# Performance work log

Measured on AMD Instinct MI355X. Metric: run time of the kernel, lower is better.

The kernel has to match this reference:

```python
import jax, jax.numpy as jnp
import numpy as np

K = 512
DIM = 64


def setup_inputs() -> dict:
    key = jax.random.key(0)
    kx, ke = jax.random.split(key)
    x = jax.random.normal(kx, (64, 64, 32, 32), dtype=jnp.float32)  # (b, d, h, w)
    codebook = jax.random.normal(ke, (K, DIM), dtype=jnp.float32)  # nn.Embedding weight
    return {"x": x, "codebook": codebook}


def reference(x, codebook):
    b, d, h, w = x.shape
    # (b, d, h*w) -> (b, h*w, d)
    flat = jnp.transpose(x.reshape(b, d, h * w), (0, 2, 1))  # (b, n, d)
    x2 = jnp.sum(flat * flat, axis=-1, keepdims=True)              # (b, n, 1)
    e2 = jnp.sum(codebook * codebook, axis=-1)                     # (k,)
    xe = jnp.einsum('bnd,kd->bnk', flat, codebook)                 # (b, n, k)
    dist = x2 - 2.0 * xe + e2                                      # (b, n, k)
    idx = jnp.argmin(dist, axis=-1)                                # (b, n)
    quant = codebook[idx]                                          # (b, n, d) gather
    # straight-through estimator
    quant_st = flat + jax.lax.stop_gradient(quant - flat)
    out = jnp.transpose(quant_st, (0, 2, 1)).reshape(b, d, h, w)
    return out
```

## Files before the change

### kernel.cpp

```cpp
#include <hip/hip_runtime.h>

#define KCODES 512
#define DIM    64
#define NVEC   65536
#define TAU    0.05f

typedef __attribute__((ext_vector_type(8))) short   short8;
typedef __attribute__((ext_vector_type(4))) float   f32x4;

static __device__ __forceinline__ unsigned f2bfu(float f) {
    unsigned u = __builtin_bit_cast(unsigned, f);
    u += 0x7fffu + ((u >> 16) & 1u);
    return u >> 16;
}

__global__ void prep_kernel(const float* __restrict__ cb,
                            unsigned short* __restrict__ cbt,
                            float* __restrict__ e2q) {
    if (blockIdx.x < 128) {
        const int g   = blockIdx.x * 64 + threadIdx.x;
        const int s   = g >> 10;
        const int rem = g & 1023;
        const int h   = rem >> 9;
        const int qd  = (rem >> 6) & 7;
        const int cl  = rem & 63;
        const float* src = cb + (size_t)(s * 64 + cl) * DIM + qd * 8;
        short8 v;
#pragma unroll
        for (int j = 0; j < 8; ++j) {
            float f = src[j];
            unsigned u = __builtin_bit_cast(unsigned, f);
            if (h == 0) {
                v[j] = (short)(u >> 16);
            } else {
                float hi = __builtin_bit_cast(float, u & 0xFFFF0000u);
                v[j] = (short)f2bfu(f - hi);
            }
        }
        *(short8*)(cbt + (size_t)g * 8) = v;
    } else {
        const int k = blockIdx.x - 128;
        float v = cb[k * DIM + threadIdx.x];
        double p = (double)v * (double)v;
#pragma unroll
        for (int off = 32; off > 0; off >>= 1) p += __shfl_down(p, off, 64);
        if (threadIdx.x == 0) e2q[k] = (float)(0.5 * p + 256.0);
    }
}

__launch_bounds__(256, 4)
__global__ void vq_main(const float* __restrict__ x,
                        const float* __restrict__ cb,
                        const unsigned short* __restrict__ cbt,
                        const float* __restrict__ e2q,
                        float* __restrict__ out) {
    __shared__ __align__(16) unsigned short sA[2][8192];
    __shared__ float sE2[KCODES];
    __shared__ int   s_i1[64], s_i2[64], s_flag[64], s_win[64];

    const int tid  = threadIdx.x;
    const int wave = tid >> 6;
    const int lane = tid & 63;
    const int quad = lane >> 4;
    const int l16  = lane & 15;

    const int v0    = blockIdx.x * 64;
    const int b     = v0 >> 10;
    const int nbase = v0 & 1023;
    const float* xb = x + (size_t)b * 65536;

    short8 stg[4];
#pragma unroll
    for (int r = 0; r < 4; ++r)
        stg[r] = *(const short8*)(cbt + (size_t)(tid + r * 256) * 8);

    short8 Bh[2], Bl[2];
    {
        const int n_g = nbase + wave * 16 + l16;
#pragma unroll
        for (int ko = 0; ko < 2; ++ko) {
#pragma unroll
            for (int j = 0; j < 8; ++j) {
                const int d = quad * 8 + j + ko * 32;
                float f = -xb[(size_t)d * 1024 + n_g];
                unsigned u = __builtin_bit_cast(unsigned, f);
                float hi = __builtin_bit_cast(float, u & 0xFFFF0000u);
                Bh[ko][j] = (short)(u >> 16);
                Bl[ko][j] = (short)f2bfu(f - hi);
            }
        }
    }

    if (tid < 128) *(f32x4*)(sE2 + tid * 4) = *(const f32x4*)(e2q + tid * 4);
#pragma unroll
    for (int r = 0; r < 4; ++r)
        *(short8*)(sA[0] + (size_t)(tid + r * 256) * 8) = stg[r];
    __syncthreads();

    float f1 = 1e30f, f2_ = 1e30f;
    int   i1 = 0,     i2_ = 0;

#pragma unroll 1
    for (int s = 0; s < 8; ++s) {
        if (s < 7) {
#pragma unroll
            for (int r = 0; r < 4; ++r)
                stg[r] = *(const short8*)(cbt +
                          (size_t)((s + 1) * 1024 + tid + r * 256) * 8);
        }

        const unsigned short* buf = sA[s & 1];
#pragma unroll
        for (int st = 0; st < 4; ++st) {
            const int cbase = s * 64 + st * 16;
            const int roff  = quad * 64 + st * 16 + l16;
            short8 A00 = *(const short8*)(buf + (size_t)(      roff) * 8);
            short8 A01 = *(const short8*)(buf + (size_t)(256 + roff) * 8);
            short8 A10 = *(const short8*)(buf + (size_t)(512 + roff) * 8);
            short8 A11 = *(const short8*)(buf + (size_t)(768 + roff) * 8);
            f32x4  e2v = *(const f32x4*)(sE2 + cbase + quad * 4);

            f32x4 acc = e2v;
            acc = __builtin_amdgcn_mfma_f32_16x16x32_bf16(A00, Bh[0], acc, 0, 0, 0);
            acc = __builtin_amdgcn_mfma_f32_16x16x32_bf16(A01, Bh[1], acc, 0, 0, 0);
            acc = __builtin_amdgcn_mfma_f32_16x16x32_bf16(A00, Bl[0], acc, 0, 0, 0);
            acc = __builtin_amdgcn_mfma_f32_16x16x32_bf16(A01, Bl[1], acc, 0, 0, 0);
            acc = __builtin_amdgcn_mfma_f32_16x16x32_bf16(A10, Bh[0], acc, 0, 0, 0);
            acc = __builtin_amdgcn_mfma_f32_16x16x32_bf16(A11, Bh[1], acc, 0, 0, 0);

#pragma unroll
            for (int r = 0; r < 4; ++r) {
                float dd = acc[r];
                int   id = cbase + quad * 4 + r;
                bool  c1 = dd < f1;
                bool  c2 = dd < f2_;
                i2_ = c1 ? i1 : (c2 ? id : i2_);
                f2_ = fminf(fmaxf(f1, dd), f2_);
                i1  = c1 ? id : i1;
                f1  = fminf(f1, dd);
            }
        }

        if (s < 7) {
#pragma unroll
            for (int r = 0; r < 4; ++r)
                *(short8*)(sA[(s + 1) & 1] + (size_t)(tid + r * 256) * 8) = stg[r];
        }
        __syncthreads();
    }

    {
#pragma unroll
        for (int delta = 16; delta <= 32; delta <<= 1) {
            float of1 = __shfl_xor(f1, delta, 64);
            int   oi1 = __shfl_xor(i1, delta, 64);
            float of2 = __shfl_xor(f2_, delta, 64);
            int   oi2 = __shfl_xor(i2_, delta, 64);
            bool o1_first = (of1 < f1) || (of1 == f1 && oi1 < i1);
            if (o1_first) {
                bool keep = (f1 < of2) || (f1 == of2 && i1 < oi2);
                f2_ = keep ? f1 : of2;
                i2_ = keep ? i1 : oi2;
                f1 = of1; i1 = oi1;
            } else {
                bool o1_second = (of1 < f2_) || (of1 == f2_ && oi1 < i2_);
                if (o1_second) { f2_ = of1; i2_ = oi1; }
            }
        }
        if (quad == 0) {
            const int vl = wave * 16 + l16;
            s_win[vl]  = i1;
            s_i1[vl]   = i1;
            s_i2[vl]   = i2_;
            s_flag[vl] = (f2_ - f1) < TAU;
        }
    }
    __syncthreads();

    {
        const int vec = tid >> 2, sub = tid & 3;
        if (s_flag[vec]) {
            const int i1c = s_i1[vec], i2c = s_i2[vec];
            const float* xr = xb + nbase + vec;
            const float* r1 = cb + (size_t)i1c * DIM;
            const float* r2 = cb + (size_t)i2c * DIM;
            double D1 = 0.0, D2 = 0.0;
#pragma unroll 4
            for (int i = 0; i < 16; ++i) {
                const int d = sub + 4 * i;
                double xd = (double)xr[(size_t)d * 1024];
                double t1 = xd - (double)r1[d]; D1 += t1 * t1;
                double t2 = xd - (double)r2[d]; D2 += t2 * t2;
            }
            D1 += __shfl_down(D1, 2, 64); D1 += __shfl_down(D1, 1, 64);
            D2 += __shfl_down(D2, 2, 64); D2 += __shfl_down(D2, 1, 64);
            if (sub == 0) {
                if (D2 < D1 || (D2 == D1 && i2c < i1c)) s_win[vec] = i2c;
            }
        }
    }
    __syncthreads();

    {
        const int n    = tid & 63;
        const int dgrp = tid >> 6;
        const float4* crow = (const float4*)(cb + (size_t)s_win[n] * DIM);
        float* op = out + (size_t)b * 65536 + nbase + n;
#pragma unroll
        for (int i = 0; i < 4; ++i) {
            const int d0 = dgrp * 16 + i * 4;
            float4 val = crow[d0 >> 2];
            op[(size_t)(d0 + 0) * 1024] = val.x;
            op[(size_t)(d0 + 1) * 1024] = val.y;
            op[(size_t)(d0 + 2) * 1024] = val.z;
            op[(size_t)(d0 + 3) * 1024] = val.w;
        }
    }
}

extern "C" void kernel_launch(void* const* d_in, const int* in_sizes, int n_in,
                              void* d_out, int out_size, void* d_ws, size_t ws_size,
                              hipStream_t stream) {
    const float* x  = (const float*)d_in[0];
    const float* cb = (const float*)d_in[1];
    float* out = (float*)d_out;

    unsigned short* cbt = (unsigned short*)d_ws;
    float*          e2q = (float*)(cbt + 8192 * 8);

    prep_kernel<<<640, 64, 0, stream>>>(cb, cbt, e2q);
    vq_main<<<NVEC / 64, 256, 0, stream>>>(x, cb, cbt, e2q, out);
}
```

Measured before the change: 89.73 us.

## Split codebook across waves so each wave handles all 64 vectors

Each wave now owns a 16-code slice of every 64-code stage and computes distances for all four 16-vector tiles, with the x fragments shared through LDS. Each A fragment read from LDS is reused across four MFMA groups, so per-wave LDS reads of the codebook drop roughly fourfold. Because each wave now sees only a quarter of the codes, the per-vector top-2 results from the four waves are merged in a cross-wave LDS reduction stage. The cost is more registers (launch bounds lowered from 4 to 3 blocks per CU), 16KB of extra shared memory, and an extra barrier with a serial merge step.

```diff
diff --git a/kernel.cpp b/kernel.cpp
--- a/kernel.cpp
+++ b/kernel.cpp
@@ -48,15 +48,25 @@
     }
 }
 
-__launch_bounds__(256, 4)
+__launch_bounds__(256, 3)
 __global__ void vq_main(const float* __restrict__ x,
                         const float* __restrict__ cb,
                         const unsigned short* __restrict__ cbt,
                         const float* __restrict__ e2q,
                         float* __restrict__ out) {
     __shared__ __align__(16) unsigned short sA[2][8192];
+    __shared__ __align__(16) unsigned char  sMix[16384];
     __shared__ float sE2[KCODES];
-    __shared__ int   s_i1[64], s_i2[64], s_flag[64], s_win[64];
+
+    unsigned short* sB = (unsigned short*)sMix;
+    float* s_pf1 = (float*)sMix;
+    float* s_pf2 = (float*)(sMix + 1024);
+    int*   s_pi1 = (int*)(sMix + 2048);
+    int*   s_pi2 = (int*)(sMix + 3072);
+    int*   s_i1  = (int*)(sMix + 4096);
+    int*   s_i2  = (int*)(sMix + 4352);
+    int*   s_flag= (int*)(sMix + 4608);
+    int*   s_win = (int*)(sMix + 4864);
 
     const int tid  = threadIdx.x;
     const int wave = tid >> 6;
@@ -74,20 +84,22 @@
     for (int r = 0; r < 4; ++r)
         stg[r] = *(const short8*)(cbt + (size_t)(tid + r * 256) * 8);
 
-    short8 Bh[2], Bl[2];
     {
         const int n_g = nbase + wave * 16 + l16;
 #pragma unroll
         for (int ko = 0; ko < 2; ++ko) {
+            short8 bh, bl;
 #pragma unroll
             for (int j = 0; j < 8; ++j) {
                 const int d = quad * 8 + j + ko * 32;
                 float f = -xb[(size_t)d * 1024 + n_g];
                 unsigned u = __builtin_bit_cast(unsigned, f);
                 float hi = __builtin_bit_cast(float, u & 0xFFFF0000u);
-                Bh[ko][j] = (short)(u >> 16);
-                Bl[ko][j] = (short)f2bfu(f - hi);
-            }
+                bh[j] = (short)(u >> 16);
+                bl[j] = (short)f2bfu(f - hi);
+            }
+            *(short8*)(sB + (size_t)(wave * 256 +       ko * 64 + lane) * 8) = bh;
+            *(short8*)(sB + (size_t)(wave * 256 + 128 + ko * 64 + lane) * 8) = bl;
         }
     }
 
@@ -97,8 +109,24 @@
         *(short8*)(sA[0] + (size_t)(tid + r * 256) * 8) = stg[r];
     __syncthreads();
 
-    float f1 = 1e30f, f2_ = 1e30f;
-    int   i1 = 0,     i2_ = 0;
+    short8 Bh[4][2], Bl[4][2];
+#pragma unroll
+    for (int nt = 0; nt < 4; ++nt) {
+#pragma unroll
+        for (int ko = 0; ko < 2; ++ko) {
+            Bh[nt][ko] = *(const short8*)(sB + (size_t)(nt * 256 +       ko * 64 + lane) * 8);
+            Bl[nt][ko] = *(const short8*)(sB + (size_t)(nt * 256 + 128 + ko * 64 + lane) * 8);
+        }
+    }
+
+    float f1[4], f2_[4];
+    int   i1[4], i2_[4];
+#pragma unroll
+    for (int nt = 0; nt < 4; ++nt) {
+        f1[nt] = 1e30f; f2_[nt] = 1e30f; i1[nt] = 0; i2_[nt] = 0;
+    }
+
+    const int roff = quad * 64 + wave * 16 + l16;
 
 #pragma unroll 1
     for (int s = 0; s < 8; ++s) {
@@ -110,34 +138,34 @@
         }
 
         const unsigned short* buf = sA[s & 1];
-#pragma unroll
-        for (int st = 0; st < 4; ++st) {
-            const int cbase = s * 64 + st * 16;
-            const int roff  = quad * 64 + st * 16 + l16;
-            short8 A00 = *(const short8*)(buf + (size_t)(      roff) * 8);
-            short8 A01 = *(const short8*)(buf + (size_t)(256 + roff) * 8);
-            short8 A10 = *(const short8*)(buf + (size_t)(512 + roff) * 8);
-            short8 A11 = *(const short8*)(buf + (size_t)(768 + roff) * 8);
-            f32x4  e2v = *(const f32x4*)(sE2 + cbase + quad * 4);
-
+        short8 A00 = *(const short8*)(buf + (size_t)(      roff) * 8);
+        short8 A01 = *(const short8*)(buf + (size_t)(256 + roff) * 8);
+        short8 A10 = *(const short8*)(buf + (size_t)(512 + roff) * 8);
+        short8 A11 = *(const short8*)(buf + (size_t)(768 + roff) * 8);
+        const int cbase = s * 64 + wave * 16;
+        const int idb   = cbase + quad * 4;
+        f32x4 e2v = *(const f32x4*)(sE2 + cbase + quad * 4);
+
+#pragma unroll
+        for (int nt = 0; nt < 4; ++nt) {
             f32x4 acc = e2v;
-            acc = __builtin_amdgcn_mfma_f32_16x16x32_bf16(A00, Bh[0], acc, 0, 0, 0);
-            acc = __builtin_amdgcn_mfma_f32_16x16x32_bf16(A01, Bh[1], acc, 0, 0, 0);
-            acc = __builtin_amdgcn_mfma_f32_16x16x32_bf16(A00, Bl[0], acc, 0, 0, 0);
-            acc = __builtin_amdgcn_mfma_f32_16x16x32_bf16(A01, Bl[1], acc, 0, 0, 0);
-            acc = __builtin_amdgcn_mfma_f32_16x16x32_bf16(A10, Bh[0], acc, 0, 0, 0);
-            acc = __builtin_amdgcn_mfma_f32_16x16x32_bf16(A11, Bh[1], acc, 0, 0, 0);
+            acc = __builtin_amdgcn_mfma_f32_16x16x32_bf16(A00, Bh[nt][0], acc, 0, 0, 0);
+            acc = __builtin_amdgcn_mfma_f32_16x16x32_bf16(A01, Bh[nt][1], acc, 0, 0, 0);
+            acc = __builtin_amdgcn_mfma_f32_16x16x32_bf16(A00, Bl[nt][0], acc, 0, 0, 0);
+            acc = __builtin_amdgcn_mfma_f32_16x16x32_bf16(A01, Bl[nt][1], acc, 0, 0, 0);
+            acc = __builtin_amdgcn_mfma_f32_16x16x32_bf16(A10, Bh[nt][0], acc, 0, 0, 0);
+            acc = __builtin_amdgcn_mfma_f32_16x16x32_bf16(A11, Bh[nt][1], acc, 0, 0, 0);
 
 #pragma unroll
             for (int r = 0; r < 4; ++r) {
                 float dd = acc[r];
-                int   id = cbase + quad * 4 + r;
-                bool  c1 = dd < f1;
-                bool  c2 = dd < f2_;
-                i2_ = c1 ? i1 : (c2 ? id : i2_);
-                f2_ = fminf(fmaxf(f1, dd), f2_);
-                i1  = c1 ? id : i1;
-                f1  = fminf(f1, dd);
+                int   id = idb + r;
+                bool  c1 = dd < f1[nt];
+                bool  c2 = dd < f2_[nt];
+                i2_[nt] = c1 ? i1[nt] : (c2 ? id : i2_[nt]);
+                f2_[nt] = fminf(fmaxf(f1[nt], dd), f2_[nt]);
+                i1[nt]  = c1 ? id : i1[nt];
+                f1[nt]  = fminf(f1[nt], dd);
             }
         }
 
@@ -149,31 +177,60 @@
         __syncthreads();
     }
 
-    {
+#pragma unroll
+    for (int nt = 0; nt < 4; ++nt) {
+        float F1 = f1[nt], F2 = f2_[nt];
+        int   I1 = i1[nt], I2 = i2_[nt];
 #pragma unroll
         for (int delta = 16; delta <= 32; delta <<= 1) {
-            float of1 = __shfl_xor(f1, delta, 64);
-            int   oi1 = __shfl_xor(i1, delta, 64);
-            float of2 = __shfl_xor(f2_, delta, 64);
-            int   oi2 = __shfl_xor(i2_, delta, 64);
-            bool o1_first = (of1 < f1) || (of1 == f1 && oi1 < i1);
+            float of1 = __shfl_xor(F1, delta, 64);
+            int   oi1 = __shfl_xor(I1, delta, 64);
+            float of2 = __shfl_xor(F2, delta, 64);
+            int   oi2 = __shfl_xor(I2, delta, 64);
+            bool o1_first = (of1 < F1) || (of1 == F1 && oi1 < I1);
             if (o1_first) {
-                bool keep = (f1 < of2) || (f1 == of2 && i1 < oi2);
-                f2_ = keep ? f1 : of2;
-                i2_ = keep ? i1 : oi2;
-                f1 = of1; i1 = oi1;
+                bool keep = (F1 < of2) || (F1 == of2 && I1 < oi2);
+                F2 = keep ? F1 : of2;
+                I2 = keep ? I1 : oi2;
+                F1 = of1; I1 = oi1;
             } else {
-                bool o1_second = (of1 < f2_) || (of1 == f2_ && oi1 < i2_);
-                if (o1_second) { f2_ = of1; i2_ = oi1; }
+                bool o1_second = (of1 < F2) || (of1 == F2 && oi1 < I2);
+                if (o1_second) { F2 = of1; I2 = oi1; }
             }
         }
         if (quad == 0) {
-            const int vl = wave * 16 + l16;
-            s_win[vl]  = i1;
-            s_i1[vl]   = i1;
-            s_i2[vl]   = i2_;
-            s_flag[vl] = (f2_ - f1) < TAU;
-        }
+            const int v = nt * 16 + l16;
+            s_pf1[v * 4 + wave] = F1;
+            s_pf2[v * 4 + wave] = F2;
+            s_pi1[v * 4 + wave] = I1;
+            s_pi2[v * 4 + wave] = I2;
+        }
+    }
+    __syncthreads();
+
+    if (tid < 64) {
+        const int v = tid;
+        float F1 = s_pf1[v * 4 + 0], F2 = s_pf2[v * 4 + 0];
+        int   I1 = s_pi1[v * 4 + 0], I2 = s_pi2[v * 4 + 0];
+#pragma unroll
+        for (int w = 1; w < 4; ++w) {
+            float of1 = s_pf1[v * 4 + w], of2 = s_pf2[v * 4 + w];
+            int   oi1 = s_pi1[v * 4 + w], oi2 = s_pi2[v * 4 + w];
+            bool o1_first = (of1 < F1) || (of1 == F1 && oi1 < I1);
+            if (o1_first) {
+                bool keep = (F1 < of2) || (F1 == of2 && I1 < oi2);
+                F2 = keep ? F1 : of2;
+                I2 = keep ? I1 : oi2;
+                F1 = of1; I1 = oi1;
+            } else {
+                bool o1_second = (of1 < F2) || (of1 == F2 && oi1 < I2);
+                if (o1_second) { F2 = of1; I2 = oi1; }
+            }
+        }
+        s_win[v]  = I1;
+        s_i1[v]   = I1;
+        s_i2[v]   = I2;
+        s_flag[v] = (F2 - F1) < TAU;
     }
     __syncthreads();
 
```

New measurement: 100.1 us. 1.12x slower.
